# Kernel tuning notes

Hardware: AMD Instinct MI355X
Metric: run time of the kernel (lower is better)

Reference implementation:

```python
import jax, jax.numpy as jnp
import numpy as np
from jax import lax

B, N, D = 8, 16384, 64
NPOINT, NSAMPLE, RADIUS = 1024, 32, 0.1
MLP = [3 + D, 64, 64, 128]
BN_EPS = 1e-5


def setup_inputs() -> dict:
    key = jax.random.key(0)
    ks = jax.random.split(key, 8)
    inp = {
        'xyz': jax.random.uniform(ks[0], (B, 3, N), dtype=jnp.float32),
        'points': jax.random.normal(ks[1], (B, D, N), dtype=jnp.float32),
    }
    for i, (cin, cout) in enumerate(zip(MLP[:-1], MLP[1:]), start=1):
        inp[f'w{i}'] = jax.random.normal(ks[1 + i], (cout, cin), dtype=jnp.float32) / np.sqrt(cin)
        inp[f'b{i}'] = jnp.zeros((cout,), jnp.float32)
        inp[f'g{i}'] = jnp.ones((cout,), jnp.float32)
        inp[f'be{i}'] = jnp.zeros((cout,), jnp.float32)
    return inp


def farthest_point_sample(xyz, npoint):
    # xyz: (B, N, 3). Deterministic start at index 0 (torch uses randint).
    b, n, _ = xyz.shape

    def step(carry, _):
        distance, farthest = carry  # (B,N), (B,)
        centroid = jnp.take_along_axis(xyz, farthest[:, None, None], axis=1)  # (B,1,3)
        dist = jnp.sum((xyz - centroid) ** 2, axis=-1)  # (B,N)
        distance = jnp.minimum(distance, dist)
        new_far = jnp.argmax(distance, axis=-1).astype(jnp.int32)
        return (distance, new_far), farthest

    init = (jnp.full((b, n), 1e10, xyz.dtype), jnp.zeros((b,), jnp.int32))
    _, idxs = lax.scan(step, init, None, length=npoint)  # (npoint, B)
    return idxs.T  # (B, npoint)


def query_ball_point(radius, nsample, xyz, new_xyz):
    # xyz: (B,N,3), new_xyz: (B,S,3) -> (B,S,nsample) int32
    b, n, _ = xyz.shape
    # squared pairwise distances (B,S,N)
    sqr = (jnp.sum(new_xyz ** 2, -1)[:, :, None]
           + jnp.sum(xyz ** 2, -1)[:, None, :]
           - 2.0 * jnp.einsum('bsc,bnc->bsn', new_xyz, xyz))
    group_idx = jnp.where(sqr > radius ** 2, n, jnp.arange(n, dtype=jnp.int32))
    group_idx = jnp.sort(group_idx, axis=-1)[:, :, :nsample]
    first = group_idx[:, :, :1]
    return jnp.where(group_idx == n, first, group_idx)


def reference(xyz, points, w1, b1, g1, be1, w2, b2, g2, be2, w3, b3, g3, be3):
    xyz_t = xyz.transpose(0, 2, 1)      # (B,N,3)
    pts_t = points.transpose(0, 2, 1)   # (B,N,D)
    bsz = xyz_t.shape[0]

    fps_idx = farthest_point_sample(xyz_t, NPOINT)          # (B,S)
    bidx2 = jnp.arange(bsz)[:, None]
    new_xyz = xyz_t[bidx2, fps_idx]                          # (B,S,3)

    idx = query_ball_point(RADIUS, NSAMPLE, xyz_t, new_xyz)  # (B,S,ns)
    bidx3 = jnp.arange(bsz)[:, None, None]
    grouped_xyz = xyz_t[bidx3, idx] - new_xyz[:, :, None, :]  # (B,S,ns,3)
    grouped_pts = pts_t[bidx3, idx]                           # (B,S,ns,D)
    feat = jnp.concatenate([grouped_xyz, grouped_pts], axis=-1)  # (B,S,ns,C)

    for w, b, g, be in ((w1, b1, g1, be1), (w2, b2, g2, be2), (w3, b3, g3, be3)):
        feat = jnp.einsum('bsnc,oc->bsno', feat, w) + b
        mean = feat.mean(axis=(0, 1, 2))
        var = feat.var(axis=(0, 1, 2))  # biased, as torch BN uses for normalization
        feat = (feat - mean) * lax.rsqrt(var + BN_EPS) * g + be
        feat = jax.nn.relu(feat)

    new_points = feat.max(axis=2)  # max over nsample -> (B,S,Cout)
    return new_xyz.transpose(0, 2, 1), new_points.transpose(0, 2, 1)
```

## Files before the change

### kernel.cpp

```cpp
#include <hip/hip_runtime.h>
#include <hip/hip_bf16.h>
#include <stdint.h>

#define BATCH 8
#define NPTS  16384
#define DIMF  64
#define SPTS  1024
#define NSAMP 32
#define MTOT  (BATCH*SPTS*NSAMP)

__device__ __forceinline__ float bfu_lo(uint32_t u){ return __uint_as_float(u<<16); }
__device__ __forceinline__ float bfu_hi(uint32_t u){ return __uint_as_float(u & 0xffff0000u); }
__device__ __forceinline__ uint16_t f2bf(float f){
  __hip_bfloat16 h = __float2bfloat16(f);
  uint16_t u; __builtin_memcpy(&u, &h, 2); return u;
}

__global__ __launch_bounds__(256) void transpose_kernel(const float* __restrict__ pts,
                                                        float* __restrict__ ptsT){
  __shared__ float tile[32][33];
  int b = blockIdx.z;
  int n0 = blockIdx.x*32, c0 = blockIdx.y*32;
  int tx = threadIdx.x & 31, ty = threadIdx.x >> 5;
  const float* src = pts + (size_t)b*DIMF*NPTS;
  float* dst = ptsT + (size_t)b*NPTS*DIMF;
#pragma unroll
  for (int j=0;j<4;j++)
    tile[ty+8*j][tx] = src[(size_t)(c0+ty+8*j)*NPTS + n0 + tx];
  __syncthreads();
#pragma unroll
  for (int j=0;j<4;j++)
    dst[(size_t)(n0+ty+8*j)*DIMF + c0 + tx] = tile[tx][ty+8*j];
}

__global__ __launch_bounds__(512, 2) void fps_kernel(const float* __restrict__ xyz,
                                                     float* __restrict__ out0){
  int b = blockIdx.x;
  const float* X = xyz + (size_t)b*3*NPTS;
  int t = threadIdx.x;
  int lane = t & 63, wid = t >> 6;
  float px[32], py[32], pz[32], dst[32];
#pragma unroll
  for (int k=0;k<32;k++){
    int n = t + (k<<9);
    px[k]=X[n]; py[k]=X[NPTS+n]; pz[k]=X[2*NPTS+n];
    dst[k]=1e10f;
  }
  __shared__ float rv[2][8];
  __shared__ int   ri[2][8];
  int far = 0;
  float* o = out0 + (size_t)b*3*SPTS;
  for (int s=0;s<SPTS;s++){
    float cx = X[far], cy = X[NPTS+far], cz = X[2*NPTS+far];
    if (t==0){ o[s]=cx; o[SPTS+s]=cy; o[2*SPTS+s]=cz; }
    if (s==SPTS-1) break;
    float best = -1.0f; int bi = 0x7fffffff;
#pragma unroll
    for (int k=0;k<32;k++){
      float dx=__fsub_rn(px[k],cx), dy=__fsub_rn(py[k],cy), dz=__fsub_rn(pz[k],cz);
      float d = __fadd_rn(__fadd_rn(__fmul_rn(dx,dx),__fmul_rn(dy,dy)),__fmul_rn(dz,dz));
      d = fminf(dst[k], d); dst[k] = d;
      if (d > best){ best = d; bi = t + (k<<9); }
    }
#pragma unroll
    for (int off=1; off<64; off<<=1){
      float ov = __shfl_xor(best, off);
      int   oi = __shfl_xor(bi, off);
      if (ov > best || (ov == best && oi < bi)){ best = ov; bi = oi; }
    }
    int p = s & 1;
    if (lane==0){ rv[p][wid]=best; ri[p][wid]=bi; }
    __syncthreads();
    float v = rv[p][lane&7]; int j = ri[p][lane&7];
#pragma unroll
    for (int off=1; off<8; off<<=1){
      float ov = __shfl_xor(v, off);
      int   oj = __shfl_xor(j, off);
      if (ov > v || (ov == v && oj < j)){ v = ov; j = oj; }
    }
    far = j;
  }
}

__global__ __launch_bounds__(256) void ball_kernel(const float* __restrict__ xyz,
                                                   const float* __restrict__ newxyz,
                                                   int* __restrict__ idxo){
  int b  = blockIdx.x >> 5;
  int sc = blockIdx.x & 31;
  const float* X  = xyz + (size_t)b*3*NPTS;
  int t = threadIdx.x, lane = t & 63, w = t >> 6;
  __shared__ float lx[512], ly[512], lz[512], ls[512];
  __shared__ int done;
  if (t==0) done = 0;
  const float rsq = 0.01f;
  float nx[8], ny[8], nz[8], sn[8];
  int cnt[8], first[8];
  int sbase = sc*32 + w*8;
#pragma unroll
  for (int q=0;q<8;q++){
    int s = sbase + q;
    nx[q] = newxyz[(size_t)b*3*SPTS + s];
    ny[q] = newxyz[(size_t)b*3*SPTS + SPTS + s];
    nz[q] = newxyz[(size_t)b*3*SPTS + 2*SPTS + s];
    sn[q] = __fadd_rn(__fadd_rn(__fmul_rn(nx[q],nx[q]),__fmul_rn(ny[q],ny[q])),
                      __fmul_rn(nz[q],nz[q]));
    cnt[q]=0; first[q]=0;
  }
  __syncthreads();
  for (int T=0;T<32;T++){
    {
      float ax = X[T*512 + t], ay = X[NPTS + T*512 + t], az = X[2*NPTS + T*512 + t];
      lx[t]=ax; ly[t]=ay; lz[t]=az;
      ls[t] = __fadd_rn(__fadd_rn(__fmul_rn(ax,ax),__fmul_rn(ay,ay)),__fmul_rn(az,az));
      float bx = X[T*512 + t + 256], by = X[NPTS + T*512 + t + 256], bz = X[2*NPTS + T*512 + t + 256];
      lx[t+256]=bx; ly[t+256]=by; lz[t+256]=bz;
      ls[t+256] = __fadd_rn(__fadd_rn(__fmul_rn(bx,bx),__fmul_rn(by,by)),__fmul_rn(bz,bz));
    }
    __syncthreads();
#pragma unroll
    for (int q=0;q<8;q++){
      if (cnt[q] >= NSAMP) continue;
      int s = sbase + q;
      int* op = idxo + ((size_t)(b*SPTS + s))*NSAMP;
      for (int c=0;c<8;c++){
        int li = c*64 + lane;
        float dot = fmaf(nz[q], lz[li], fmaf(ny[q], ly[li], __fmul_rn(nx[q], lx[li])));
        float sq  = __fsub_rn(__fadd_rn(sn[q], ls[li]), __fmul_rn(2.0f, dot));
        bool in = (sq <= rsq);
        unsigned long long m = __ballot(in);
        if (cnt[q]==0 && m) first[q] = T*512 + c*64 + (int)__builtin_ctzll(m);
        if (in){
          int slot = cnt[q] + (int)__popcll(m & ((1ull<<lane)-1ull));
          if (slot < NSAMP) op[slot] = T*512 + li;
        }
        cnt[q] += (int)__popcll(m);
        if (cnt[q] >= NSAMP){ if (lane==0) atomicAdd(&done,1); break; }
      }
    }
    __syncthreads();
    if (done >= 32) break;
  }
#pragma unroll
  for (int q=0;q<8;q++){
    if (cnt[q] < NSAMP){
      int s = sbase + q;
      int* op = idxo + ((size_t)(b*SPTS + s))*NSAMP;
      if (lane >= cnt[q] && lane < NSAMP) op[lane] = first[q];
    }
  }
}

__global__ __launch_bounds__(256) void gemm1_kernel(const float* __restrict__ xyz,
                                                    const float* __restrict__ ptsT,
                                                    const int* __restrict__ idx,
                                                    const float* __restrict__ newxyz,
                                                    const float* __restrict__ w1,
                                                    const float* __restrict__ b1,
                                                    uint16_t* __restrict__ y1){
  __shared__ float As[128*69];
  __shared__ float Ws[67*64];
  __shared__ float bias[64];
  __shared__ int   ndx[128];
  __shared__ float nxs[4][3];
  int t = threadIdx.x;
  int g0 = blockIdx.x*128;
  if (t < 128) ndx[t] = idx[g0 + t];
  if (t < 12){
    int grp = t/3, c = t%3;
    int bs = (g0>>5) + grp; int b = bs>>10, s = bs & 1023;
    nxs[grp][c] = newxyz[(size_t)b*3*SPTS + c*SPTS + s];
  }
  if (t < 64) bias[t] = b1[t];
  for (int e=t; e<67*64; e+=256){ int k=e>>6, c=e&63; Ws[k*64+c] = w1[c*67+k]; }
  __syncthreads();
  {
    int r = t>>1, h = t&1;
    int n = ndx[r];
    int bs = (g0>>5) + (r>>5); int b = bs>>10;
    const float* pr = ptsT + ((size_t)(b*NPTS + n))*64 + h*32;
    float* ar = As + r*69;
    if (h==0){
      int grp = r>>5;
      ar[0] = __fsub_rn(xyz[(size_t)b*3*NPTS + n],          nxs[grp][0]);
      ar[1] = __fsub_rn(xyz[(size_t)b*3*NPTS + NPTS + n],   nxs[grp][1]);
      ar[2] = __fsub_rn(xyz[(size_t)b*3*NPTS + 2*NPTS + n], nxs[grp][2]);
    }
    float* ap = ar + 3 + h*32;
#pragma unroll
    for (int j=0;j<8;j++){
      float4 v = *(const float4*)(pr + j*4);
      ap[j*4+0]=v.x; ap[j*4+1]=v.y; ap[j*4+2]=v.z; ap[j*4+3]=v.w;
    }
  }
  __syncthreads();
  int rg = t>>3, cg = t&7;
  float acc[4][8];
#pragma unroll
  for (int i=0;i<4;i++)
#pragma unroll
    for (int j=0;j<8;j++) acc[i][j]=0.f;
  for (int k=0;k<67;k++){
    float a0 = As[(rg*4+0)*69+k];
    float a1 = As[(rg*4+1)*69+k];
    float a2 = As[(rg*4+2)*69+k];
    float a3 = As[(rg*4+3)*69+k];
    const float* wr = Ws + k*64 + cg*8;
    float4 w0 = *(const float4*)wr;
    float4 w1v = *(const float4*)(wr+4);
    float wj[8] = {w0.x,w0.y,w0.z,w0.w,w1v.x,w1v.y,w1v.z,w1v.w};
#pragma unroll
    for (int j=0;j<8;j++){
      acc[0][j] = fmaf(a0, wj[j], acc[0][j]);
      acc[1][j] = fmaf(a1, wj[j], acc[1][j]);
      acc[2][j] = fmaf(a2, wj[j], acc[2][j]);
      acc[3][j] = fmaf(a3, wj[j], acc[3][j]);
    }
  }
#pragma unroll
  for (int i=0;i<4;i++){
    int gr = g0 + rg*4 + i;
    uint16_t* yr = y1 + (size_t)gr*64 + cg*8;
    uint4 vv;
    uint32_t u[4];
#pragma unroll
    for (int j=0;j<4;j++){
      float v0 = acc[i][2*j]   + bias[cg*8+2*j];
      float v1 = acc[i][2*j+1] + bias[cg*8+2*j+1];
      u[j] = (uint32_t)f2bf(v0) | ((uint32_t)f2bf(v1)<<16);
    }
    vv.x=u[0]; vv.y=u[1]; vv.z=u[2]; vv.w=u[3];
    *(uint4*)yr = vv;
  }
}

__global__ __launch_bounds__(256) void gemm2_kernel(const uint16_t* __restrict__ yin,
                                                    const float* __restrict__ w2,
                                                    const float* __restrict__ b2,
                                                    const float* __restrict__ scale,
                                                    const float* __restrict__ shift,
                                                    uint16_t* __restrict__ yout){
  __shared__ float As[128*65];
  __shared__ float Ws[64*64];
  __shared__ float bias[64], sc[64], sh[64];
  int t = threadIdx.x;
  int g0 = blockIdx.x*128;
  if (t < 64){ bias[t]=b2[t]; sc[t]=scale[t]; sh[t]=shift[t]; }
  for (int e=t; e<64*64; e+=256){ int k=e>>6, c=e&63; Ws[k*64+c] = w2[c*64+k]; }
  __syncthreads();
  {
    int r = t>>1, h = t&1;
    const uint4* yv = (const uint4*)(yin + (size_t)(g0+r)*64 + h*32);
    float* ar = As + r*65 + h*32;
#pragma unroll
    for (int j=0;j<4;j++){
      uint4 u = yv[j];
      uint32_t vv[4] = {u.x,u.y,u.z,u.w};
#pragma unroll
      for (int m=0;m<4;m++){
        int c = h*32 + j*8 + m*2;
        ar[j*8+m*2]   = fmaxf(fmaf(bfu_lo(vv[m]), sc[c],   sh[c]),   0.f);
        ar[j*8+m*2+1] = fmaxf(fmaf(bfu_hi(vv[m]), sc[c+1], sh[c+1]), 0.f);
      }
    }
  }
  __syncthreads();
  int rg = t>>3, cg = t&7;
  float acc[4][8];
#pragma unroll
  for (int i=0;i<4;i++)
#pragma unroll
    for (int j=0;j<8;j++) acc[i][j]=0.f;
  for (int k=0;k<64;k++){
    float a0 = As[(rg*4+0)*65+k];
    float a1 = As[(rg*4+1)*65+k];
    float a2 = As[(rg*4+2)*65+k];
    float a3 = As[(rg*4+3)*65+k];
    const float* wr = Ws + k*64 + cg*8;
    float4 w0 = *(const float4*)wr;
    float4 w1v = *(const float4*)(wr+4);
    float wj[8] = {w0.x,w0.y,w0.z,w0.w,w1v.x,w1v.y,w1v.z,w1v.w};
#pragma unroll
    for (int j=0;j<8;j++){
      acc[0][j] = fmaf(a0, wj[j], acc[0][j]);
      acc[1][j] = fmaf(a1, wj[j], acc[1][j]);
      acc[2][j] = fmaf(a2, wj[j], acc[2][j]);
      acc[3][j] = fmaf(a3, wj[j], acc[3][j]);
    }
  }
#pragma unroll
  for (int i=0;i<4;i++){
    int gr = g0 + rg*4 + i;
    uint16_t* yr = yout + (size_t)gr*64 + cg*8;
    uint4 vv; uint32_t u[4];
#pragma unroll
    for (int j=0;j<4;j++){
      float v0 = acc[i][2*j]   + bias[cg*8+2*j];
      float v1 = acc[i][2*j+1] + bias[cg*8+2*j+1];
      u[j] = (uint32_t)f2bf(v0) | ((uint32_t)f2bf(v1)<<16);
    }
    vv.x=u[0]; vv.y=u[1]; vv.z=u[2]; vv.w=u[3];
    *(uint4*)yr = vv;
  }
}

__global__ __launch_bounds__(256) void gemm3_kernel(const uint16_t* __restrict__ yin,
                                                    const float* __restrict__ w3,
                                                    const float* __restrict__ b3,
                                                    const float* __restrict__ scale,
                                                    const float* __restrict__ shift,
                                                    uint16_t* __restrict__ yout){
  __shared__ float As[64*65];
  __shared__ float Ws[64*128];
  __shared__ float bias[128], sc[64], sh[64];
  int t = threadIdx.x;
  int g0 = blockIdx.x*64;
  if (t < 128) bias[t]=b3[t];
  if (t < 64){ sc[t]=scale[t]; sh[t]=shift[t]; }
  for (int e=t; e<64*128; e+=256){ int k=e>>7, c=e&127; Ws[k*128+c] = w3[c*64+k]; }
  __syncthreads();
  {
    int r = t>>2, h = t&3;
    const uint4* yv = (const uint4*)(yin + (size_t)(g0+r)*64 + h*16);
    float* ar = As + r*65 + h*16;
#pragma unroll
    for (int j=0;j<2;j++){
      uint4 u = yv[j];
      uint32_t vv[4] = {u.x,u.y,u.z,u.w};
#pragma unroll
      for (int m=0;m<4;m++){
        int c = h*16 + j*8 + m*2;
        ar[j*8+m*2]   = fmaxf(fmaf(bfu_lo(vv[m]), sc[c],   sh[c]),   0.f);
        ar[j*8+m*2+1] = fmaxf(fmaf(bfu_hi(vv[m]), sc[c+1], sh[c+1]), 0.f);
      }
    }
  }
  __syncthreads();
  int rg = t>>4, cg = t&15;
  float acc[4][8];
#pragma unroll
  for (int i=0;i<4;i++)
#pragma unroll
    for (int j=0;j<8;j++) acc[i][j]=0.f;
  for (int k=0;k<64;k++){
    float a0 = As[(rg*4+0)*65+k];
    float a1 = As[(rg*4+1)*65+k];
    float a2 = As[(rg*4+2)*65+k];
    float a3 = As[(rg*4+3)*65+k];
    const float* wr = Ws + k*128 + cg*8;
    float4 w0 = *(const float4*)wr;
    float4 w1v = *(const float4*)(wr+4);
    float wj[8] = {w0.x,w0.y,w0.z,w0.w,w1v.x,w1v.y,w1v.z,w1v.w};
#pragma unroll
    for (int j=0;j<8;j++){
      acc[0][j] = fmaf(a0, wj[j], acc[0][j]);
      acc[1][j] = fmaf(a1, wj[j], acc[1][j]);
      acc[2][j] = fmaf(a2, wj[j], acc[2][j]);
      acc[3][j] = fmaf(a3, wj[j], acc[3][j]);
    }
  }
#pragma unroll
  for (int i=0;i<4;i++){
    int gr = g0 + rg*4 + i;
    uint16_t* yr = yout + (size_t)gr*128 + cg*8;
    uint4 vv; uint32_t u[4];
#pragma unroll
    for (int j=0;j<4;j++){
      float v0 = acc[i][2*j]   + bias[cg*8+2*j];
      float v1 = acc[i][2*j+1] + bias[cg*8+2*j+1];
      u[j] = (uint32_t)f2bf(v0) | ((uint32_t)f2bf(v1)<<16);
    }
    vv.x=u[0]; vv.y=u[1]; vv.z=u[2]; vv.w=u[3];
    *(uint4*)yr = vv;
  }
}

template<int C>
__global__ __launch_bounds__(256) void stats_kernel(const uint16_t* __restrict__ y,
                                                    float* __restrict__ gsum,
                                                    float* __restrict__ gsq){
  constexpr int CP  = C/2;
  constexpr int RSL = 256/CP;
  int t = threadIdx.x;
  int c0 = t % CP, rs = t / CP;
  float s0=0.f,q0=0.f,s1=0.f,q1=0.f;
#pragma unroll 4
  for (int i=0;i<512/RSL;i++){
    int r = blockIdx.x*512 + rs + i*RSL;
    uint32_t u = *(const uint32_t*)(y + (size_t)r*C + 2*c0);
    float v0 = bfu_lo(u), v1 = bfu_hi(u);
    s0 += v0; q0 += v0*v0; s1 += v1; q1 += v1*v1;
  }
  __shared__ float red[4][256];
  red[0][t]=s0; red[1][t]=q0; red[2][t]=s1; red[3][t]=q1;
  __syncthreads();
  if (t < CP){
    float a0=0,a1=0,a2=0,a3=0;
    for (int k=0;k<RSL;k++){
      a0+=red[0][k*CP+t]; a1+=red[1][k*CP+t]; a2+=red[2][k*CP+t]; a3+=red[3][k*CP+t];
    }
    atomicAdd(&gsum[2*t],   a0); atomicAdd(&gsq[2*t],   a1);
    atomicAdd(&gsum[2*t+1], a2); atomicAdd(&gsq[2*t+1], a3);
  }
}

__global__ void finalize_kernel(const float* __restrict__ gsum, const float* __restrict__ gsq,
                                const float* __restrict__ g, const float* __restrict__ be,
                                float* __restrict__ scale, float* __restrict__ shift, int C){
  int c = threadIdx.x;
  if (c >= C) return;
  double mean = (double)gsum[c] / (double)MTOT;
  double var  = (double)gsq[c] / (double)MTOT - mean*mean;
  double s    = (double)g[c] / sqrt(var + 1e-5);
  scale[c] = (float)s;
  shift[c] = (float)((double)be[c] - mean*s);
}

__global__ __launch_bounds__(256) void maxpool_kernel(const uint16_t* __restrict__ y3,
                                                      const float* __restrict__ scale,
                                                      const float* __restrict__ shift,
                                                      float* __restrict__ out1){
  __shared__ float tr[16][129];
  int t = threadIdx.x;
  int b = blockIdx.x >> 6;
  int s0 = (blockIdx.x & 63) * 16;
  int ch = t & 127, sl0 = t >> 7;
  float scv = scale[ch], shv = shift[ch];
  for (int sl=sl0; sl<16; sl+=2){
    int bs = b*SPTS + s0 + sl;
    const uint16_t* yr = y3 + (size_t)bs*NSAMP*128 + ch;
    float m = 0.0f;
#pragma unroll 4
    for (int k=0;k<NSAMP;k++){
      float v = __uint_as_float(((uint32_t)yr[k*128])<<16);
      float z = fmaxf(fmaf(v, scv, shv), 0.f);
      m = fmaxf(m, z);
    }
    tr[sl][ch] = m;
  }
  __syncthreads();
  int ch2 = t >> 1, hh = t & 1;
  float vals[8];
#pragma unroll
  for (int i=0;i<8;i++) vals[i] = tr[hh*8+i][ch2];
  float* op = out1 + (size_t)b*131072 + (size_t)ch2*1024 + s0 + hh*8;
  float4 v0; v0.x=vals[0]; v0.y=vals[1]; v0.z=vals[2]; v0.w=vals[3];
  float4 v1; v1.x=vals[4]; v1.y=vals[5]; v1.z=vals[6]; v1.w=vals[7];
  *(float4*)op = v0;
  *(float4*)(op+4) = v1;
}

extern "C" void kernel_launch(void* const* d_in, const int* in_sizes, int n_in,
                              void* d_out, int out_size, void* d_ws, size_t ws_size,
                              hipStream_t stream){
  (void)in_sizes; (void)n_in; (void)out_size; (void)ws_size;
  const float* xyz = (const float*)d_in[0];
  const float* pts = (const float*)d_in[1];
  const float* w1 = (const float*)d_in[2];  const float* b1 = (const float*)d_in[3];
  const float* g1 = (const float*)d_in[4];  const float* be1 = (const float*)d_in[5];
  const float* w2 = (const float*)d_in[6];  const float* b2 = (const float*)d_in[7];
  const float* g2 = (const float*)d_in[8];  const float* be2 = (const float*)d_in[9];
  const float* w3 = (const float*)d_in[10]; const float* b3 = (const float*)d_in[11];
  const float* g3 = (const float*)d_in[12]; const float* be3 = (const float*)d_in[13];

  float* out0 = (float*)d_out;
  float* out1 = out0 + BATCH*3*SPTS;

  char* ws = (char*)d_ws;
  float*    ptsT = (float*)(ws + 0);
  int*      idx  = (int*)  (ws + 34078720);
  uint16_t* y1   = (uint16_t*)(ws + 35127296);
  uint16_t* y2   = (uint16_t*)(ws + 68681728);
  uint16_t* y3   = (uint16_t*)(ws + 102236160);
  float*    stats = (float*)(ws + 169345024);
  float* gsum1 = stats;        float* gsq1 = stats + 128;
  float* gsum2 = stats + 256;  float* gsq2 = stats + 384;
  float* gsum3 = stats + 512;  float* gsq3 = stats + 640;
  float* scale1 = stats + 768; float* shift1 = stats + 896;
  float* scale2 = stats + 1024; float* shift2 = stats + 1152;
  float* scale3 = stats + 1280; float* shift3 = stats + 1408;

  hipMemsetAsync(stats, 0, 768*sizeof(float), stream);

  transpose_kernel<<<dim3(NPTS/32, DIMF/32, BATCH), 256, 0, stream>>>(pts, ptsT);
  fps_kernel<<<BATCH, 512, 0, stream>>>(xyz, out0);
  ball_kernel<<<BATCH*32, 256, 0, stream>>>(xyz, out0, idx);
  gemm1_kernel<<<MTOT/128, 256, 0, stream>>>(xyz, ptsT, idx, out0, w1, b1, y1);
  stats_kernel<64><<<512, 256, 0, stream>>>(y1, gsum1, gsq1);
  finalize_kernel<<<1, 128, 0, stream>>>(gsum1, gsq1, g1, be1, scale1, shift1, 64);
  gemm2_kernel<<<MTOT/128, 256, 0, stream>>>(y1, w2, b2, scale1, shift1, y2);
  stats_kernel<64><<<512, 256, 0, stream>>>(y2, gsum2, gsq2);
  finalize_kernel<<<1, 128, 0, stream>>>(gsum2, gsq2, g2, be2, scale2, shift2, 64);
  gemm3_kernel<<<MTOT/64, 256, 0, stream>>>(y2, w3, b3, scale2, shift2, y3);
  stats_kernel<128><<<512, 256, 0, stream>>>(y3, gsum3, gsq3);
  finalize_kernel<<<1, 128, 0, stream>>>(gsum3, gsq3, g3, be3, scale3, shift3, 128);
  maxpool_kernel<<<BATCH*(SPTS/16), 256, 0, stream>>>(y3, scale3, shift3, out1);
}
```

Before: 2.642 ms.

## Fuse BatchNorm statistics into GEMM epilogues and finalize into consumers

Each GEMM now accumulates per-channel sum and sum-of-squares from its fp32 outputs in registers, reduces them in shared memory, and atomically adds them to the global stats. The separate stats and finalize kernels are removed, and scale/shift are computed in double at the start of each consumer kernel. This removes three full re-reads of the bf16 activations and six kernel launches. In exchange, every GEMM block does extra reduction work and global atomics. Stats are now taken from pre-rounding fp32 values rather than bf16, which slightly changes numerics.

```diff
diff --git a/kernel.cpp b/kernel.cpp
--- a/kernel.cpp
+++ b/kernel.cpp
@@ -156,7 +156,9 @@
                                                     const float* __restrict__ newxyz,
                                                     const float* __restrict__ w1,
                                                     const float* __restrict__ b1,
-                                                    uint16_t* __restrict__ y1){
+                                                    uint16_t* __restrict__ y1,
+                                                    float* __restrict__ gsum,
+                                                    float* __restrict__ gsq){
   __shared__ float As[128*69];
   __shared__ float Ws[67*64];
   __shared__ float bias[64];
@@ -216,35 +218,63 @@
       acc[3][j] = fmaf(a3, wj[j], acc[3][j]);
     }
   }
+  float ps[8], pq[8];
+#pragma unroll
+  for (int j=0;j<8;j++){ ps[j]=0.f; pq[j]=0.f; }
 #pragma unroll
   for (int i=0;i<4;i++){
     int gr = g0 + rg*4 + i;
     uint16_t* yr = y1 + (size_t)gr*64 + cg*8;
-    uint4 vv;
-    uint32_t u[4];
-#pragma unroll
-    for (int j=0;j<4;j++){
-      float v0 = acc[i][2*j]   + bias[cg*8+2*j];
-      float v1 = acc[i][2*j+1] + bias[cg*8+2*j+1];
-      u[j] = (uint32_t)f2bf(v0) | ((uint32_t)f2bf(v1)<<16);
-    }
+    uint4 vv; uint32_t u[4]; float vj[8];
+#pragma unroll
+    for (int j=0;j<8;j++){
+      vj[j] = acc[i][j] + bias[cg*8+j];
+      ps[j] += vj[j]; pq[j] += vj[j]*vj[j];
+    }
+#pragma unroll
+    for (int j=0;j<4;j++)
+      u[j] = (uint32_t)f2bf(vj[2*j]) | ((uint32_t)f2bf(vj[2*j+1])<<16);
     vv.x=u[0]; vv.y=u[1]; vv.z=u[2]; vv.w=u[3];
     *(uint4*)yr = vv;
+  }
+  __syncthreads();
+  float* red = As;
+#pragma unroll
+  for (int j=0;j<8;j++){
+    red[rg*65 + cg*8 + j]        = ps[j];
+    red[2080 + rg*65 + cg*8 + j] = pq[j];
+  }
+  __syncthreads();
+  if (t < 64){
+    float s=0.f, q=0.f;
+    for (int r=0;r<32;r++){ s += red[r*65+t]; q += red[2080 + r*65 + t]; }
+    atomicAdd(&gsum[t], s); atomicAdd(&gsq[t], q);
   }
 }
 
 __global__ __launch_bounds__(256) void gemm2_kernel(const uint16_t* __restrict__ yin,
                                                     const float* __restrict__ w2,
                                                     const float* __restrict__ b2,
-                                                    const float* __restrict__ scale,
-                                                    const float* __restrict__ shift,
-                                                    uint16_t* __restrict__ yout){
+                                                    const float* __restrict__ gsumi,
+                                                    const float* __restrict__ gsqi,
+                                                    const float* __restrict__ gi,
+                                                    const float* __restrict__ bei,
+                                                    uint16_t* __restrict__ yout,
+                                                    float* __restrict__ gsum,
+                                                    float* __restrict__ gsq){
   __shared__ float As[128*65];
   __shared__ float Ws[64*64];
   __shared__ float bias[64], sc[64], sh[64];
   int t = threadIdx.x;
   int g0 = blockIdx.x*128;
-  if (t < 64){ bias[t]=b2[t]; sc[t]=scale[t]; sh[t]=shift[t]; }
+  if (t < 64){
+    bias[t]=b2[t];
+    double mean = (double)gsumi[t] / (double)MTOT;
+    double var  = (double)gsqi[t] / (double)MTOT - mean*mean;
+    double sv   = (double)gi[t] / sqrt(var + 1e-5);
+    sc[t] = (float)sv;
+    sh[t] = (float)((double)bei[t] - mean*sv);
+  }
   for (int e=t; e<64*64; e+=256){ int k=e>>6, c=e&63; Ws[k*64+c] = w2[c*64+k]; }
   __syncthreads();
   {
@@ -287,35 +317,63 @@
       acc[3][j] = fmaf(a3, wj[j], acc[3][j]);
     }
   }
+  float ps[8], pq[8];
+#pragma unroll
+  for (int j=0;j<8;j++){ ps[j]=0.f; pq[j]=0.f; }
 #pragma unroll
   for (int i=0;i<4;i++){
     int gr = g0 + rg*4 + i;
     uint16_t* yr = yout + (size_t)gr*64 + cg*8;
-    uint4 vv; uint32_t u[4];
-#pragma unroll
-    for (int j=0;j<4;j++){
-      float v0 = acc[i][2*j]   + bias[cg*8+2*j];
-      float v1 = acc[i][2*j+1] + bias[cg*8+2*j+1];
-      u[j] = (uint32_t)f2bf(v0) | ((uint32_t)f2bf(v1)<<16);
-    }
+    uint4 vv; uint32_t u[4]; float vj[8];
+#pragma unroll
+    for (int j=0;j<8;j++){
+      vj[j] = acc[i][j] + bias[cg*8+j];
+      ps[j] += vj[j]; pq[j] += vj[j]*vj[j];
+    }
+#pragma unroll
+    for (int j=0;j<4;j++)
+      u[j] = (uint32_t)f2bf(vj[2*j]) | ((uint32_t)f2bf(vj[2*j+1])<<16);
     vv.x=u[0]; vv.y=u[1]; vv.z=u[2]; vv.w=u[3];
     *(uint4*)yr = vv;
+  }
+  __syncthreads();
+  float* red = As;
+#pragma unroll
+  for (int j=0;j<8;j++){
+    red[rg*65 + cg*8 + j]        = ps[j];
+    red[2080 + rg*65 + cg*8 + j] = pq[j];
+  }
+  __syncthreads();
+  if (t < 64){
+    float s=0.f, q=0.f;
+    for (int r=0;r<32;r++){ s += red[r*65+t]; q += red[2080 + r*65 + t]; }
+    atomicAdd(&gsum[t], s); atomicAdd(&gsq[t], q);
   }
 }
 
 __global__ __launch_bounds__(256) void gemm3_kernel(const uint16_t* __restrict__ yin,
                                                     const float* __restrict__ w3,
                                                     const float* __restrict__ b3,
-                                                    const float* __restrict__ scale,
-                                                    const float* __restrict__ shift,
-                                                    uint16_t* __restrict__ yout){
+                                                    const float* __restrict__ gsumi,
+                                                    const float* __restrict__ gsqi,
+                                                    const float* __restrict__ gi,
+                                                    const float* __restrict__ bei,
+                                                    uint16_t* __restrict__ yout,
+                                                    float* __restrict__ gsum,
+                                                    float* __restrict__ gsq){
   __shared__ float As[64*65];
   __shared__ float Ws[64*128];
   __shared__ float bias[128], sc[64], sh[64];
   int t = threadIdx.x;
   int g0 = blockIdx.x*64;
   if (t < 128) bias[t]=b3[t];
-  if (t < 64){ sc[t]=scale[t]; sh[t]=shift[t]; }
+  if (t < 64){
+    double mean = (double)gsumi[t] / (double)MTOT;
+    double var  = (double)gsqi[t] / (double)MTOT - mean*mean;
+    double sv   = (double)gi[t] / sqrt(var + 1e-5);
+    sc[t] = (float)sv;
+    sh[t] = (float)((double)bei[t] - mean*sv);
+  }
   for (int e=t; e<64*128; e+=256){ int k=e>>7, c=e&127; Ws[k*128+c] = w3[c*64+k]; }
   __syncthreads();
   {
@@ -358,73 +416,61 @@
       acc[3][j] = fmaf(a3, wj[j], acc[3][j]);
     }
   }
+  float ps[8], pq[8];
+#pragma unroll
+  for (int j=0;j<8;j++){ ps[j]=0.f; pq[j]=0.f; }
 #pragma unroll
   for (int i=0;i<4;i++){
     int gr = g0 + rg*4 + i;
     uint16_t* yr = yout + (size_t)gr*128 + cg*8;
-    uint4 vv; uint32_t u[4];
-#pragma unroll
-    for (int j=0;j<4;j++){
-      float v0 = acc[i][2*j]   + bias[cg*8+2*j];
-      float v1 = acc[i][2*j+1] + bias[cg*8+2*j+1];
-      u[j] = (uint32_t)f2bf(v0) | ((uint32_t)f2bf(v1)<<16);
-    }
+    uint4 vv; uint32_t u[4]; float vj[8];
+#pragma unroll
+    for (int j=0;j<8;j++){
+      vj[j] = acc[i][j] + bias[cg*8+j];
+      ps[j] += vj[j]; pq[j] += vj[j]*vj[j];
+    }
+#pragma unroll
+    for (int j=0;j<4;j++)
+      u[j] = (uint32_t)f2bf(vj[2*j]) | ((uint32_t)f2bf(vj[2*j+1])<<16);
     vv.x=u[0]; vv.y=u[1]; vv.z=u[2]; vv.w=u[3];
     *(uint4*)yr = vv;
   }
-}
-
-template<int C>
-__global__ __launch_bounds__(256) void stats_kernel(const uint16_t* __restrict__ y,
-                                                    float* __restrict__ gsum,
-                                                    float* __restrict__ gsq){
-  constexpr int CP  = C/2;
-  constexpr int RSL = 256/CP;
-  int t = threadIdx.x;
-  int c0 = t % CP, rs = t / CP;
-  float s0=0.f,q0=0.f,s1=0.f,q1=0.f;
-#pragma unroll 4
-  for (int i=0;i<512/RSL;i++){
-    int r = blockIdx.x*512 + rs + i*RSL;
-    uint32_t u = *(const uint32_t*)(y + (size_t)r*C + 2*c0);
-    float v0 = bfu_lo(u), v1 = bfu_hi(u);
-    s0 += v0; q0 += v0*v0; s1 += v1; q1 += v1*v1;
-  }
-  __shared__ float red[4][256];
-  red[0][t]=s0; red[1][t]=q0; red[2][t]=s1; red[3][t]=q1;
-  __syncthreads();
-  if (t < CP){
-    float a0=0,a1=0,a2=0,a3=0;
-    for (int k=0;k<RSL;k++){
-      a0+=red[0][k*CP+t]; a1+=red[1][k*CP+t]; a2+=red[2][k*CP+t]; a3+=red[3][k*CP+t];
-    }
-    atomicAdd(&gsum[2*t],   a0); atomicAdd(&gsq[2*t],   a1);
-    atomicAdd(&gsum[2*t+1], a2); atomicAdd(&gsq[2*t+1], a3);
-  }
-}
-
-__global__ void finalize_kernel(const float* __restrict__ gsum, const float* __restrict__ gsq,
-                                const float* __restrict__ g, const float* __restrict__ be,
-                                float* __restrict__ scale, float* __restrict__ shift, int C){
-  int c = threadIdx.x;
-  if (c >= C) return;
-  double mean = (double)gsum[c] / (double)MTOT;
-  double var  = (double)gsq[c] / (double)MTOT - mean*mean;
-  double s    = (double)g[c] / sqrt(var + 1e-5);
-  scale[c] = (float)s;
-  shift[c] = (float)((double)be[c] - mean*s);
+  __syncthreads();
+  float* red = As;
+#pragma unroll
+  for (int j=0;j<8;j++){
+    red[rg*129 + cg*8 + j]        = ps[j];
+    red[2064 + rg*129 + cg*8 + j] = pq[j];
+  }
+  __syncthreads();
+  if (t < 128){
+    float s=0.f, q=0.f;
+    for (int r=0;r<16;r++){ s += red[r*129+t]; q += red[2064 + r*129 + t]; }
+    atomicAdd(&gsum[t], s); atomicAdd(&gsq[t], q);
+  }
 }
 
 __global__ __launch_bounds__(256) void maxpool_kernel(const uint16_t* __restrict__ y3,
-                                                      const float* __restrict__ scale,
-                                                      const float* __restrict__ shift,
+                                                      const float* __restrict__ gsumi,
+                                                      const float* __restrict__ gsqi,
+                                                      const float* __restrict__ gi,
+                                                      const float* __restrict__ bei,
                                                       float* __restrict__ out1){
   __shared__ float tr[16][129];
+  __shared__ float scs[128], shs[128];
   int t = threadIdx.x;
   int b = blockIdx.x >> 6;
   int s0 = (blockIdx.x & 63) * 16;
+  if (t < 128){
+    double mean = (double)gsumi[t] / (double)MTOT;
+    double var  = (double)gsqi[t] / (double)MTOT - mean*mean;
+    double sv   = (double)gi[t] / sqrt(var + 1e-5);
+    scs[t] = (float)sv;
+    shs[t] = (float)((double)bei[t] - mean*sv);
+  }
+  __syncthreads();
   int ch = t & 127, sl0 = t >> 7;
-  float scv = scale[ch], shv = shift[ch];
+  float scv = scs[ch], shv = shs[ch];
   for (int sl=sl0; sl<16; sl+=2){
     int bs = b*SPTS + s0 + sl;
     const uint16_t* yr = y3 + (size_t)bs*NSAMP*128 + ch;
@@ -475,23 +521,14 @@
   float* gsum1 = stats;        float* gsq1 = stats + 128;
   float* gsum2 = stats + 256;  float* gsq2 = stats + 384;
   float* gsum3 = stats + 512;  float* gsq3 = stats + 640;
-  float* scale1 = stats + 768; float* shift1 = stats + 896;
-  float* scale2 = stats + 1024; float* shift2 = stats + 1152;
-  float* scale3 = stats + 1280; float* shift3 = stats + 1408;
 
   hipMemsetAsync(stats, 0, 768*sizeof(float), stream);
 
   transpose_kernel<<<dim3(NPTS/32, DIMF/32, BATCH), 256, 0, stream>>>(pts, ptsT);
   fps_kernel<<<BATCH, 512, 0, stream>>>(xyz, out0);
   ball_kernel<<<BATCH*32, 256, 0, stream>>>(xyz, out0, idx);
-  gemm1_kernel<<<MTOT/128, 256, 0, stream>>>(xyz, ptsT, idx, out0, w1, b1, y1);
-  stats_kernel<64><<<512, 256, 0, stream>>>(y1, gsum1, gsq1);
-  finalize_kernel<<<1, 128, 0, stream>>>(gsum1, gsq1, g1, be1, scale1, shift1, 64);
-  gemm2_kernel<<<MTOT/128, 256, 0, stream>>>(y1, w2, b2, scale1, shift1, y2);
-  stats_kernel<64><<<512, 256, 0, stream>>>(y2, gsum2, gsq2);
-  finalize_kernel<<<1, 128, 0, stream>>>(gsum2, gsq2, g2, be2, scale2, shift2, 64);
-  gemm3_kernel<<<MTOT/64, 256, 0, stream>>>(y2, w3, b3, scale2, shift2, y3);
-  stats_kernel<128><<<512, 256, 0, stream>>>(y3, gsum3, gsq3);
-  finalize_kernel<<<1, 128, 0, stream>>>(gsum3, gsq3, g3, be3, scale3, shift3, 128);
-  maxpool_kernel<<<BATCH*(SPTS/16), 256, 0, stream>>>(y3, scale3, shift3, out1);
-}
+  gemm1_kernel<<<MTOT/128, 256, 0, stream>>>(xyz, ptsT, idx, out0, w1, b1, y1, gsum1, gsq1);
+  gemm2_kernel<<<MTOT/128, 256, 0, stream>>>(y1, w2, b2, gsum1, gsq1, g1, be1, y2, gsum2, gsq2);
+  gemm3_kernel<<<MTOT/64, 256, 0, stream>>>(y2, w3, b3, gsum2, gsq2, g2, be2, y3, gsum3, gsq3);
+  maxpool_kernel<<<BATCH*(SPTS/16), 256, 0, stream>>>(y3, gsum3, gsq3, g3, be3, out1);
+}
```

After: 2.660 ms. About the same (+0.7%).
